# Performance work log

Measured on AMD Instinct MI355X. Metric: run time of the kernel, lower is better.

## Reference

```python
import jax, jax.numpy as jnp
import numpy as np

B, S, D = 4, 2048, 2048
H = 16
NOPE, ROPE, VD = 128, 64, 128
QK = NOPE + ROPE            # 192 per-head q/k dim
KVR = 512                   # kv_lora_rank
THETA = 10000.0
EPS = 1e-6
SCALE = QK ** -0.5


def _freqs(seq_len, d, theta):
    inv = 1.0 / (theta ** (np.arange(0, d, 2, dtype=np.float64) / d))
    ang = np.outer(np.arange(seq_len, dtype=np.float64), inv)  # [S, d//2]
    return jnp.asarray(np.cos(ang), jnp.float32), jnp.asarray(np.sin(ang), jnp.float32)


def apply_rope(x, cos, sin):
    # x: [B, S, H, d]; cos/sin: [S, d//2]; complex multiply on (even, odd) pairs
    xr = x.reshape(*x.shape[:-1], -1, 2)
    xe, xo = xr[..., 0], xr[..., 1]
    c = cos[None, :, None, :]
    s = sin[None, :, None, :]
    ye = xe * c - xo * s
    yo = xe * s + xo * c
    return jnp.stack([ye, yo], axis=-1).reshape(x.shape)


def rmsnorm(x, w, eps=EPS):
    return x * jax.lax.rsqrt(jnp.mean(x * x, axis=-1, keepdims=True) + eps) * w


def setup_inputs() -> dict:
    key = jax.random.key(0)
    ks = jax.random.split(key, 6)
    sd = 0.02
    x = jax.random.normal(ks[0], (B, S, D), jnp.float32)
    wq = jax.random.normal(ks[1], (H * QK, D), jnp.float32) * sd
    wkv_a = jax.random.normal(ks[2], (KVR + ROPE, D), jnp.float32) * sd
    kv_norm_w = jnp.ones((KVR,), jnp.float32)
    wkv_b = jax.random.normal(ks[3], (H * (NOPE + VD), KVR), jnp.float32) * sd
    wo = jax.random.normal(ks[4], (D, H * VD), jnp.float32) * sd
    cos, sin = _freqs(S, ROPE, THETA)
    return {"x": x, "wq": wq, "wkv_a": wkv_a, "kv_norm_w": kv_norm_w,
            "wkv_b": wkv_b, "wo": wo, "freqs_cos": cos, "freqs_sin": sin}


def reference(x, wq, wkv_a, kv_norm_w, wkv_b, wo, freqs_cos, freqs_sin):
    b, s, _ = x.shape
    # query projection (q_lora_rank == 0 path)
    q = jnp.einsum('bsd,ed->bse', x, wq).reshape(b, s, H, QK)
    q_nope, q_pe = q[..., :NOPE], q[..., NOPE:]
    q_pe = apply_rope(q_pe, freqs_cos, freqs_sin)

    # low-rank KV latent + decoupled rope key
    kv = jnp.einsum('bsd,ed->bse', x, wkv_a)          # [b,s,KVR+ROPE]
    kv_c, k_pe = kv[..., :KVR], kv[..., KVR:]
    k_pe = apply_rope(k_pe[:, :, None, :], freqs_cos, freqs_sin)  # [b,s,1,ROPE]
    kv_c = rmsnorm(kv_c, kv_norm_w)
    kvb = jnp.einsum('bsr,er->bse', kv_c, wkv_b).reshape(b, s, H, NOPE + VD)
    k_nope, v = kvb[..., :NOPE], kvb[..., NOPE:]
    k = jnp.concatenate([k_nope, jnp.broadcast_to(k_pe, (b, s, H, ROPE))], axis=-1)
    q_full = jnp.concatenate([q_nope, q_pe], axis=-1)

    # causal attention
    scores = jnp.einsum('bqhd,bkhd->bhqk', q_full, k) * SCALE
    mask = jnp.triu(jnp.full((s, s), -jnp.inf, jnp.float32), k=1)
    scores = scores + mask[None, None]
    p = jax.nn.softmax(scores, axis=-1)
    out = jnp.einsum('bhqk,bkhd->bqhd', p, v).reshape(b, s, H * VD)
    return jnp.einsum('bse,de->bsd', out, wo)
```

## Files before the change

### kernel.cpp

```cpp
#include <hip/hip_runtime.h>
#include <math.h>

#define BB 4
#define SS 2048
#define DD 2048
#define HH 16
#define NOPE 128
#define ROPE 64
#define VD 128
#define QKD 192
#define KVR 512
#define NP1 3712
#define ROWS (BB*SS)
#define SCL2 0.1041216338380858f

typedef __attribute__((ext_vector_type(8))) short bf16x8;
typedef __attribute__((ext_vector_type(4))) float f32x4;
typedef unsigned short bfu;
typedef __attribute__((address_space(1))) const void GV;
typedef __attribute__((address_space(3))) void LV;

__device__ __forceinline__ float bf2f(unsigned int u) {
    unsigned int i = u << 16; float f; __builtin_memcpy(&f, &i, 4); return f;
}
__device__ __forceinline__ unsigned int f2bf(float f) {
    unsigned int i; __builtin_memcpy(&i, &f, 4);
    return (i + 0x7fffu + ((i >> 16) & 1u)) >> 16;
}
__device__ __forceinline__ unsigned int cvt_pk_bf16(float lo, float hi) {
    unsigned int r;
    asm("v_cvt_pk_bf16_f32 %0, %1, %2" : "=v"(r) : "v"(lo), "v"(hi));
    return r;
}

__global__ void cast_f32_bf16(const float* __restrict__ src, bfu* __restrict__ dst,
                              long n_src, long n_dst) {
    long i = (long)blockIdx.x * blockDim.x + threadIdx.x;
    if (i * 4 >= n_dst) return;
    unsigned int lo = 0, hi = 0;
    if (i * 4 < n_src) {
        float4 v = ((const float4*)src)[i];
        lo = f2bf(v.x) | (f2bf(v.y) << 16);
        hi = f2bf(v.z) | (f2bf(v.w) << 16);
    }
    ((uint2*)dst)[i] = make_uint2(lo, hi);
}

__global__ void cast_weights(const float* __restrict__ wq, const float* __restrict__ wa,
                             const float* __restrict__ wb, const float* __restrict__ wo,
                             bfu* __restrict__ dq, bfu* __restrict__ da,
                             bfu* __restrict__ db, bfu* __restrict__ dwo) {
    long i = (long)blockIdx.x * 256 + threadIdx.x;
    const float* src; bfu* dst; long off, n_src; float scl = 1.0f;
    if (i < 1572864L)        { src = wq; dst = dq;  off = i;            n_src = 1572864L; scl = SCL2; }
    else if (i < 1900544L)   { src = wa; dst = da;  off = i - 1572864L; n_src = 294912L;  }
    else if (i < 2424832L)   { src = wb; dst = db;  off = i - 1900544L; n_src = 524288L;  }
    else if (i < 3473408L)   { src = wo; dst = dwo; off = i - 2424832L; n_src = 1048576L; }
    else return;
    unsigned int lo = 0, hi = 0;
    if (off < n_src) {
        float4 v = ((const float4*)src)[off];
        lo = f2bf(v.x * scl) | (f2bf(v.y * scl) << 16);
        hi = f2bf(v.z * scl) | (f2bf(v.w * scl) << 16);
    }
    ((uint2*)dst)[off] = make_uint2(lo, hi);
}

template <int MODE>
__global__ void __launch_bounds__(256)
gemm_bt(const bfu* __restrict__ A, const bfu* __restrict__ Bt,
        void* __restrict__ Cv, bfu* __restrict__ C2, int N, int K) {
    __shared__ __align__(16) char lds[32768];
    char* AsB = lds;
    char* BsB = lds + 16384;
    const int tid  = threadIdx.x;
    const int lane = tid & 63;
    const int wid  = tid >> 6;
    const int wr   = wid >> 1, wc = wid & 1;
    const long m0 = (long)blockIdx.y * 128;
    const long n0 = (long)blockIdx.x * 128;

    f32x4 acc[4][4] = {};

    const int lr = lane >> 3;
    const int SB = (lane & 7) << 4;

    for (int k0 = 0; k0 < K; k0 += 64) {
        __syncthreads();
#pragma unroll
        for (int i = 0; i < 4; ++i) {
            int rb = wid * 32 + i * 8;
            int R  = rb + lr;
            int c  = (SB ^ ((R & 7) << 4)) >> 1;
            const bfu* gA = A  + (m0 + R) * (long)K + k0 + c;
            const bfu* gB = Bt + (n0 + R) * (long)K + k0 + c;
            __builtin_amdgcn_global_load_lds((GV*)gA, (LV*)(AsB + rb * 128), 16, 0, 0);
            __builtin_amdgcn_global_load_lds((GV*)gB, (LV*)(BsB + rb * 128), 16, 0, 0);
        }
        __syncthreads();
#pragma unroll
        for (int kk = 0; kk < 2; ++kk) {
            bf16x8 av[4], bv[4];
            const int cb = kk * 64 + ((lane >> 4) << 4);
#pragma unroll
            for (int m = 0; m < 4; ++m) {
                int R = wr * 64 + m * 16 + (lane & 15);
                av[m] = *(const bf16x8*)(AsB + R * 128 + (cb ^ ((R & 7) << 4)));
            }
#pragma unroll
            for (int n = 0; n < 4; ++n) {
                int R = wc * 64 + n * 16 + (lane & 15);
                bv[n] = *(const bf16x8*)(BsB + R * 128 + (cb ^ ((R & 7) << 4)));
            }
#pragma unroll
            for (int m = 0; m < 4; ++m)
#pragma unroll
                for (int n = 0; n < 4; ++n)
                    acc[m][n] = __builtin_amdgcn_mfma_f32_16x16x32_bf16(av[m], bv[n], acc[m][n], 0, 0, 0);
        }
    }

    const int cr = (lane >> 4) << 2;
    const int cc = lane & 15;
#pragma unroll
    for (int m = 0; m < 4; ++m)
#pragma unroll
        for (int n = 0; n < 4; ++n)
#pragma unroll
            for (int r = 0; r < 4; ++r) {
                long row = m0 + wr * 64 + m * 16 + cr + r;
                long col = n0 + wc * 64 + n * 16 + cc;
                float val = acc[m][n][r];
                if (MODE == 1) {
                    ((float*)Cv)[row * N + col] = val;
                } else if (MODE == 0) {
                    ((bfu*)Cv)[row * N + col] = (bfu)f2bf(val);
                } else {
                    long b_ = row >> 11;
                    long s  = row & 2047;
                    long h  = col >> 8;
                    long wi = col & 255;
                    if (wi < 128)
                        C2[((b_ * HH + h) * SS + s) * (long)QKD + wi] = (bfu)f2bf(val);
                    else
                        ((bfu*)Cv)[row * 2048 + h * 128 + (wi - 128)] = (bfu)f2bf(val);
                }
            }
}

__global__ void rope_q(const bfu* __restrict__ p1, bfu* __restrict__ qr,
                       const float* __restrict__ fc, const float* __restrict__ fs) {
    long t = (long)blockIdx.x * 256 + threadIdx.x;
    int  ch = (int)(t % 24);
    long r  = t / 24;
    int  s  = (int)(r & 2047);
    long bh = r >> 11;
    long b_ = bh >> 4;
    int  h  = (int)(bh & 15);
    const bfu* src = p1 + (b_ * SS + s) * (long)NP1 + h * QKD + ch * 8;
    bfu* dst = qr + (bh * SS + s) * (long)QKD + ch * 8;
    bf16x8 v = *(const bf16x8*)src;
    if (ch >= 16) {
        int i0 = (ch - 16) * 4;
        unsigned int out[4];
#pragma unroll
        for (int k = 0; k < 4; ++k) {
            float e = bf2f((unsigned short)v[2 * k]);
            float o = bf2f((unsigned short)v[2 * k + 1]);
            float c = fc[s * 32 + i0 + k], sn = fs[s * 32 + i0 + k];
            out[k] = cvt_pk_bf16(e * c - o * sn, e * sn + o * c);
        }
        uint4 u = make_uint4(out[0], out[1], out[2], out[3]);
        *(uint4*)dst = u;
    } else {
        *(bf16x8*)dst = v;
    }
}

__global__ void __launch_bounds__(256)
rms_rope_kv(const bfu* __restrict__ p1, const float* __restrict__ wn,
            bfu* __restrict__ kvc, bfu* __restrict__ kpe,
            const float* __restrict__ fc, const float* __restrict__ fs) {
    const int row = blockIdx.x;
    const int t   = threadIdx.x;
    const int s   = row & (SS - 1);
    const long base = (long)row * NP1 + 3072;
    unsigned int v = *(const unsigned int*)(p1 + base + 2 * t);
    float a = bf2f(v & 0xffff), c2 = bf2f(v >> 16);
    float ssum = a * a + c2 * c2;
#pragma unroll
    for (int d = 1; d < 64; d <<= 1) ssum += __shfl_xor(ssum, d);
    __shared__ float red[4];
    const int lane = t & 63, w = t >> 6;
    if (lane == 0) red[w] = ssum;
    __syncthreads();
    float tot = red[0] + red[1] + red[2] + red[3];
    float scale = rsqrtf(tot * (1.0f / 512.0f) + 1e-6f);
    float w0 = wn[2 * t], w1 = wn[2 * t + 1];
    unsigned int out = f2bf(a * scale * w0) | (f2bf(c2 * scale * w1) << 16);
    *(unsigned int*)(kvc + (long)row * KVR + 2 * t) = out;
    if (t < 32) {
        unsigned int pv = *(const unsigned int*)(p1 + base + KVR + 2 * t);
        float e = bf2f(pv & 0xffff), o = bf2f(pv >> 16);
        float cc = fc[s * 32 + t], sn = fs[s * 32 + t];
        unsigned int po = f2bf(e * cc - o * sn) | (f2bf(e * sn + o * cc) << 16);
        *(unsigned int*)(kpe + (long)row * ROPE + 2 * t) = po;
    }
}

__global__ void pe_fill(const bfu* __restrict__ kpe, bfu* __restrict__ kall) {
    long t = (long)blockIdx.x * 256 + threadIdx.x;
    int  ch = (int)(t & 7);
    long r  = t >> 3;
    int  s  = (int)(r & 2047);
    long bh = r >> 11;
    long b_ = bh >> 4;
    bf16x8 v = *(const bf16x8*)(kpe + (b_ * SS + s) * (long)ROPE + ch * 8);
    *(bf16x8*)(kall + (bh * SS + s) * (long)QKD + NOPE + ch * 8) = v;
}

__global__ void __launch_bounds__(256)
transpose_v2(const bfu* __restrict__ vpack, bfu* __restrict__ vt) {
    __shared__ __align__(16) char tile[64 * 256];
    const int tid = threadIdx.x;
    const int bid = blockIdx.x;
    const int st  = bid & 31;
    const int bh  = bid >> 5;
    const int h   = bh & 15;
    const long b_ = bh >> 4;
    const long sbase = b_ * SS + st * 64;
#pragma unroll
    for (int i = 0; i < 4; ++i) {
        int idx = i * 256 + tid;
        int row = idx >> 4;
        int ch  = (idx & 15) ^ ((row >> 3) & 7);
        const bfu* src = vpack + (sbase + row) * 2048 + h * 128 + ch * 8;
        __builtin_amdgcn_global_load_lds((GV*)src, (LV*)(tile + idx * 16), 16, 0, 0);
    }
    __syncthreads();
#pragma unroll
    for (int i = 0; i < 4; ++i) {
        int idx = i * 256 + tid;
        int sc = idx & 7;
        int v  = (idx >> 3) & 127;
        bfu tmp[8];
#pragma unroll
        for (int k = 0; k < 8; ++k) {
            int row = sc * 8 + k;
            tmp[k] = *(const bfu*)(tile + row * 256 + (((v >> 3) ^ ((row >> 3) & 7)) << 4) + (v & 7) * 2);
        }
        *(bf16x8*)(vt + ((long)bh * VD + v) * SS + st * 64 + sc * 8) = *(bf16x8*)tmp;
    }
}

__device__ __forceinline__ void attn_tile64(
    const char* kbuf, const char* vbuf, char* pw,
    const bf16x8 (&qf)[6], f32x4 (&accv)[8],
    float& ms, float& ls, int kv0, int qa, int ql, int kg, int lane) {
    f32x4 sc[4] = {};
#pragma unroll
    for (int j = 0; j < 4; ++j)
#pragma unroll
        for (int d = 0; d < 6; ++d) {
            int row  = j * 16 + ql;
            int slot = (d * 4 + kg) ^ (ql & 7);
            bf16x8 kf = *(const bf16x8*)(kbuf + row * 384 + slot * 16);
            sc[j] = __builtin_amdgcn_mfma_f32_16x16x32_bf16(kf, qf[d], sc[j], 0, 0, 0);
        }
    float p[4][4];
    float mx = -1e30f;
#pragma unroll
    for (int j = 0; j < 4; ++j)
#pragma unroll
        for (int r = 0; r < 4; ++r) {
            float s = sc[j][r];
            int kv = kv0 + j * 16 + kg * 4 + r;
            s = (kv > qa) ? -1e30f : s;
            p[j][r] = s;
            mx = fmaxf(mx, s);
        }
    mx = fmaxf(mx, __shfl_xor(mx, 16));
    mx = fmaxf(mx, __shfl_xor(mx, 32));
    float rs = 0.f;
    if (__all(mx <= ms)) {
#pragma unroll
        for (int j = 0; j < 4; ++j)
#pragma unroll
            for (int r = 0; r < 4; ++r) {
                float e = exp2f(p[j][r] - ms);
                p[j][r] = e;
                rs += e;
            }
        rs += __shfl_xor(rs, 16);
        rs += __shfl_xor(rs, 32);
        ls += rs;
    } else {
        float mn = fmaxf(ms, mx);
        float al = exp2f(ms - mn);
        ms = mn;
#pragma unroll
        for (int j = 0; j < 4; ++j)
#pragma unroll
            for (int r = 0; r < 4; ++r) {
                float e = exp2f(p[j][r] - mn);
                p[j][r] = e;
                rs += e;
            }
        rs += __shfl_xor(rs, 16);
        rs += __shfl_xor(rs, 32);
        ls = ls * al + rs;
        float alT[4];
#pragma unroll
        for (int r = 0; r < 4; ++r)
            alT[r] = __shfl(al, (lane & 48) + kg * 4 + r);
#pragma unroll
        for (int v8 = 0; v8 < 8; ++v8)
#pragma unroll
            for (int r = 0; r < 4; ++r)
                accv[v8][r] *= alT[r];
    }
#pragma unroll
    for (int j = 0; j < 4; ++j) {
        uint2 u;
        u.x = cvt_pk_bf16(p[j][0], p[j][1]);
        u.y = cvt_pk_bf16(p[j][2], p[j][3]);
        int slot = (2 * j + (kg >> 1)) ^ (ql & 7);
        *(uint2*)(pw + ql * 128 + slot * 16 + (kg & 1) * 8) = u;
    }
    asm volatile("s_waitcnt lgkmcnt(0)" ::: "memory");
#pragma unroll
    for (int t2 = 0; t2 < 2; ++t2) {
        int ps = (t2 * 4 + kg) ^ (ql & 7);
        bf16x8 pa = *(const bf16x8*)(pw + ql * 128 + ps * 16);
#pragma unroll
        for (int v8 = 0; v8 < 8; ++v8) {
            int vrow = v8 * 16 + ql;
            int vs   = (t2 * 4 + kg) ^ (ql & 7);
            bf16x8 vf = *(const bf16x8*)(vbuf + vrow * 128 + vs * 16);
            accv[v8] = __builtin_amdgcn_mfma_f32_16x16x32_bf16(pa, vf, accv[v8], 0, 0, 0);
        }
    }
}

__global__ void __launch_bounds__(512)
attn(const bfu* __restrict__ qr, const bfu* __restrict__ kall,
     const bfu* __restrict__ vt, bfu* __restrict__ ao) {
    __shared__ __align__(16) char kbuf[64 * 384];
    __shared__ __align__(16) char vbuf[128 * 128];
    __shared__ __align__(16) char pbuf[8][2048];
    const int tid  = threadIdx.x;
    const int lane = tid & 63;
    const int w    = tid >> 6;
    const int ql   = lane & 15;
    const int kg   = lane >> 4;
    const int bid  = blockIdx.x;
    const int qb   = 15 - (bid >> 6);
    const int bh   = bid & 63;
    const int h    = bh & 15;
    const int b    = bh >> 4;
    const char* Q  = (const char*)(qr + (long)bh * SS * QKD);
    const char* Kp = (const char*)(kall + (long)bh * SS * QKD);
    const char* Vp = (const char*)(vt + (long)bh * VD * SS);
    char* pw = pbuf[w];

    const int qa_min = qb * 128 + w * 16;
    const int qa = qa_min + ql;

    bf16x8 qf[6];
#pragma unroll
    for (int d = 0; d < 6; ++d)
        qf[d] = *(const bf16x8*)(Q + (long)(qa_min + ql) * 384 + d * 64 + kg * 16);

    f32x4 accv[8] = {};
    float ms = -1e30f, ls = 0.f;
    const int ntiles = 2 * qb + 2;

    for (int t = 0; t < ntiles; ++t) {
        const int kv0 = t * 64;
        __syncthreads();
#pragma unroll
        for (int i = 0; i < 3; ++i) {
            int idx  = i * 512 + tid;
            int row  = idx / 24;
            int slot = idx - row * 24;
            int ss   = slot ^ (row & 7);
            const char* src = Kp + (long)(kv0 + row) * 384 + ss * 16;
            __builtin_amdgcn_global_load_lds((GV*)src, (LV*)(kbuf + idx * 16), 16, 0, 0);
        }
#pragma unroll
        for (int i = 0; i < 2; ++i) {
            int idx  = i * 512 + tid;
            int row  = idx >> 3;
            int slot = idx & 7;
            int ss   = slot ^ (row & 7);
            const char* src = Vp + (long)row * (SS * 2) + kv0 * 2 + ss * 16;
            __builtin_amdgcn_global_load_lds((GV*)src, (LV*)(vbuf + idx * 16), 16, 0, 0);
        }
        __syncthreads();
        if (kv0 <= qa_min + 15)
            attn_tile64(kbuf, vbuf, pw, qf, accv, ms, ls, kv0, qa, ql, kg, lane);
    }
    float li[4];
#pragma unroll
    for (int r = 0; r < 4; ++r)
        li[r] = 1.0f / __shfl(ls, (lane & 48) + kg * 4 + r);
#pragma unroll
    for (int v8 = 0; v8 < 8; ++v8)
#pragma unroll
        for (int r = 0; r < 4; ++r) {
            float o = accv[v8][r] * li[r];
            long row = (long)b * SS + qa_min + kg * 4 + r;
            ao[row * (long)(HH * VD) + h * VD + v8 * 16 + ql] = (bfu)f2bf(o);
        }
}

#define O_XB   0L
#define O_WQ   33554432L
#define O_WA   46137344L
#define O_WB   48758784L
#define O_WO   52953088L
#define O_P1   61341696L
#define O_QR   122159104L
#define O_KVC  172490752L
#define O_KPE  180879360L
#define O_AO   181927936L
#define WS_NEED 215482368L

extern "C" void kernel_launch(void* const* d_in, const int* in_sizes, int n_in,
                              void* d_out, int out_size, void* d_ws, size_t ws_size,
                              hipStream_t stream) {
    const float* x      = (const float*)d_in[0];
    const float* wq     = (const float*)d_in[1];
    const float* wkv_a  = (const float*)d_in[2];
    const float* kvnw   = (const float*)d_in[3];
    const float* wkv_b  = (const float*)d_in[4];
    const float* wo     = (const float*)d_in[5];
    const float* fcos   = (const float*)d_in[6];
    const float* fsin   = (const float*)d_in[7];
    if (ws_size < (size_t)WS_NEED) return;

    char* ws = (char*)d_ws;
    bfu* xb   = (bfu*)(ws + O_XB);
    bfu* wqb  = (bfu*)(ws + O_WQ);
    bfu* wab  = (bfu*)(ws + O_WA);
    bfu* wbb  = (bfu*)(ws + O_WB);
    bfu* wob  = (bfu*)(ws + O_WO);
    bfu* p1   = (bfu*)(ws + O_P1);
    bfu* qr   = (bfu*)(ws + O_QR);
    bfu* kvc  = (bfu*)(ws + O_KVC);
    bfu* kpe  = (bfu*)(ws + O_KPE);
    bfu* ao   = (bfu*)(ws + O_AO);
    bfu* kall = p1;
    bfu* vt   = xb;
    bfu* vpack = (bfu*)d_out;

    cast_f32_bf16<<<16384, 256, 0, stream>>>(x, xb, 16777216L, 16777216L);
    cast_weights<<<13568, 256, 0, stream>>>(wq, wkv_a, wkv_b, wo, wqb, wab, wbb, wob);

    gemm_bt<0><<<dim3(29, 64), 256, 0, stream>>>(xb, wqb, p1, nullptr, NP1, DD);

    rope_q<<<12288, 256, 0, stream>>>(p1, qr, fcos, fsin);
    rms_rope_kv<<<ROWS, 256, 0, stream>>>(p1, kvnw, kvc, kpe, fcos, fsin);

    gemm_bt<2><<<dim3(32, 64), 256, 0, stream>>>(kvc, wbb, vpack, kall, HH * 256, KVR);

    pe_fill<<<4096, 256, 0, stream>>>(kpe, kall);
    transpose_v2<<<2048, 256, 0, stream>>>(vpack, vt);

    attn<<<1024, 512, 0, stream>>>(qr, kall, vt, ao);

    gemm_bt<1><<<dim3(16, 64), 256, 0, stream>>>(ao, wob, d_out, nullptr, DD, HH * VD);
}
```

Measured before the change: 524.8 us.

## Double-buffer attention K/V tiles at 32-key granularity and swizzle GEMM block order

The attention loop moves from a single 64-key K/V buffer, loaded and then fully synchronised, to two 32-key buffers. The next tile's global-to-LDS loads are issued before the current tile is computed, with vmcnt waits and raw barriers in place of __syncthreads. Separately, the GEMM remaps its flat block index so that groups of neighbouring workgroups share A/B tiles in cache. The smaller tiles double the number of barriers and softmax rescale steps per query block. The vmcnt counts are hand-tuned and depend on how many loads each wave issues.

Result: slower. 569.9 us (+8.6%).

```diff
diff --git a/kernel.cpp b/kernel.cpp
--- a/kernel.cpp
+++ b/kernel.cpp
@@ -77,8 +77,11 @@
     const int lane = tid & 63;
     const int wid  = tid >> 6;
     const int wr   = wid >> 1, wc = wid & 1;
-    const long m0 = (long)blockIdx.y * 128;
-    const long n0 = (long)blockIdx.x * 128;
+    const int nwg  = gridDim.x * gridDim.y;
+    const int flat = blockIdx.y * gridDim.x + blockIdx.x;
+    const int swz  = (flat & 7) * (nwg >> 3) + (flat >> 3);
+    const long m0 = (long)(swz / gridDim.x) * 128;
+    const long n0 = (long)(swz % gridDim.x) * 128;
 
     f32x4 acc[4][4] = {};
 
@@ -253,24 +256,24 @@
     }
 }
 
-__device__ __forceinline__ void attn_tile64(
-    const char* kbuf, const char* vbuf, char* pw,
+__device__ __forceinline__ void attn_tile32(
+    const char* kb, const char* vb, char* pw,
     const bf16x8 (&qf)[6], f32x4 (&accv)[8],
     float& ms, float& ls, int kv0, int qa, int ql, int kg, int lane) {
-    f32x4 sc[4] = {};
-#pragma unroll
-    for (int j = 0; j < 4; ++j)
+    f32x4 sc[2] = {};
+#pragma unroll
+    for (int j = 0; j < 2; ++j)
 #pragma unroll
         for (int d = 0; d < 6; ++d) {
             int row  = j * 16 + ql;
             int slot = (d * 4 + kg) ^ (ql & 7);
-            bf16x8 kf = *(const bf16x8*)(kbuf + row * 384 + slot * 16);
+            bf16x8 kf = *(const bf16x8*)(kb + row * 384 + slot * 16);
             sc[j] = __builtin_amdgcn_mfma_f32_16x16x32_bf16(kf, qf[d], sc[j], 0, 0, 0);
         }
-    float p[4][4];
+    float p[2][4];
     float mx = -1e30f;
 #pragma unroll
-    for (int j = 0; j < 4; ++j)
+    for (int j = 0; j < 2; ++j)
 #pragma unroll
         for (int r = 0; r < 4; ++r) {
             float s = sc[j][r];
@@ -284,7 +287,7 @@
     float rs = 0.f;
     if (__all(mx <= ms)) {
 #pragma unroll
-        for (int j = 0; j < 4; ++j)
+        for (int j = 0; j < 2; ++j)
 #pragma unroll
             for (int r = 0; r < 4; ++r) {
                 float e = exp2f(p[j][r] - ms);
@@ -299,7 +302,7 @@
         float al = exp2f(ms - mn);
         ms = mn;
 #pragma unroll
-        for (int j = 0; j < 4; ++j)
+        for (int j = 0; j < 2; ++j)
 #pragma unroll
             for (int r = 0; r < 4; ++r) {
                 float e = exp2f(p[j][r] - mn);
@@ -320,34 +323,29 @@
                 accv[v8][r] *= alT[r];
     }
 #pragma unroll
-    for (int j = 0; j < 4; ++j) {
+    for (int j = 0; j < 2; ++j) {
         uint2 u;
         u.x = cvt_pk_bf16(p[j][0], p[j][1]);
         u.y = cvt_pk_bf16(p[j][2], p[j][3]);
-        int slot = (2 * j + (kg >> 1)) ^ (ql & 7);
-        *(uint2*)(pw + ql * 128 + slot * 16 + (kg & 1) * 8) = u;
+        int un = (j * 2 + (kg >> 1)) ^ (ql & 3);
+        *(uint2*)(pw + ql * 64 + un * 16 + (kg & 1) * 8) = u;
     }
     asm volatile("s_waitcnt lgkmcnt(0)" ::: "memory");
-#pragma unroll
-    for (int t2 = 0; t2 < 2; ++t2) {
-        int ps = (t2 * 4 + kg) ^ (ql & 7);
-        bf16x8 pa = *(const bf16x8*)(pw + ql * 128 + ps * 16);
-#pragma unroll
-        for (int v8 = 0; v8 < 8; ++v8) {
-            int vrow = v8 * 16 + ql;
-            int vs   = (t2 * 4 + kg) ^ (ql & 7);
-            bf16x8 vf = *(const bf16x8*)(vbuf + vrow * 128 + vs * 16);
-            accv[v8] = __builtin_amdgcn_mfma_f32_16x16x32_bf16(pa, vf, accv[v8], 0, 0, 0);
-        }
+    bf16x8 pa = *(const bf16x8*)(pw + ql * 64 + (kg ^ (ql & 3)) * 16);
+#pragma unroll
+    for (int v8 = 0; v8 < 8; ++v8) {
+        int vrow = v8 * 16 + ql;
+        bf16x8 vf = *(const bf16x8*)(vb + vrow * 64 + ((kg ^ (ql & 3)) << 4));
+        accv[v8] = __builtin_amdgcn_mfma_f32_16x16x32_bf16(pa, vf, accv[v8], 0, 0, 0);
     }
 }
 
 __global__ void __launch_bounds__(512)
 attn(const bfu* __restrict__ qr, const bfu* __restrict__ kall,
      const bfu* __restrict__ vt, bfu* __restrict__ ao) {
-    __shared__ __align__(16) char kbuf[64 * 384];
-    __shared__ __align__(16) char vbuf[128 * 128];
-    __shared__ __align__(16) char pbuf[8][2048];
+    __shared__ __align__(16) char kbuf[2][32 * 384];
+    __shared__ __align__(16) char vbuf[2][128 * 64];
+    __shared__ __align__(16) char pbuf[8][1024];
     const int tid  = threadIdx.x;
     const int lane = tid & 63;
     const int w    = tid >> 6;
@@ -365,6 +363,26 @@
 
     const int qa_min = qb * 128 + w * 16;
     const int qa = qa_min + ql;
+    const int tlast = (qa_min + 15) >> 5;
+
+    const int kr1 = tid / 24, ks1 = tid - kr1 * 24;
+    const char* kbase1 = Kp + kr1 * 384 + (ks1 ^ (kr1 & 7)) * 16;
+    const int kdst1 = tid * 16;
+    const int ki2 = 512 + tid;
+    const int kr2 = ki2 / 24, ks2 = ki2 - kr2 * 24;
+    const char* kbase2 = Kp + kr2 * 384 + (ks2 ^ (kr2 & 7)) * 16;
+    const int kdst2 = ki2 * 16;
+    const int vr = tid >> 2, vs = tid & 3;
+    const char* vbase = Vp + (long)vr * (SS * 2) + (vs ^ (vr & 3)) * 16;
+    const int vdst = tid * 16;
+    const bool second_k = (w < 4);
+
+    auto stage = [&](int bi, long kv0) {
+        __builtin_amdgcn_global_load_lds((GV*)(kbase1 + kv0 * 384), (LV*)(kbuf[bi] + kdst1), 16, 0, 0);
+        if (second_k)
+            __builtin_amdgcn_global_load_lds((GV*)(kbase2 + kv0 * 384), (LV*)(kbuf[bi] + kdst2), 16, 0, 0);
+        __builtin_amdgcn_global_load_lds((GV*)(vbase + kv0 * 2), (LV*)(vbuf[bi] + vdst), 16, 0, 0);
+    };
 
     bf16x8 qf[6];
 #pragma unroll
@@ -373,32 +391,25 @@
 
     f32x4 accv[8] = {};
     float ms = -1e30f, ls = 0.f;
-    const int ntiles = 2 * qb + 2;
-
+    const int ntiles = 4 * qb + 4;
+
+    stage(0, 0);
     for (int t = 0; t < ntiles; ++t) {
-        const int kv0 = t * 64;
-        __syncthreads();
-#pragma unroll
-        for (int i = 0; i < 3; ++i) {
-            int idx  = i * 512 + tid;
-            int row  = idx / 24;
-            int slot = idx - row * 24;
-            int ss   = slot ^ (row & 7);
-            const char* src = Kp + (long)(kv0 + row) * 384 + ss * 16;
-            __builtin_amdgcn_global_load_lds((GV*)src, (LV*)(kbuf + idx * 16), 16, 0, 0);
-        }
-#pragma unroll
-        for (int i = 0; i < 2; ++i) {
-            int idx  = i * 512 + tid;
-            int row  = idx >> 3;
-            int slot = idx & 7;
-            int ss   = slot ^ (row & 7);
-            const char* src = Vp + (long)row * (SS * 2) + kv0 * 2 + ss * 16;
-            __builtin_amdgcn_global_load_lds((GV*)src, (LV*)(vbuf + idx * 16), 16, 0, 0);
-        }
-        __syncthreads();
-        if (kv0 <= qa_min + 15)
-            attn_tile64(kbuf, vbuf, pw, qf, accv, ms, ls, kv0, qa, ql, kg, lane);
+        const int cur = t & 1;
+        const int kv0 = t * 32;
+        if (t + 1 < ntiles) {
+            stage(cur ^ 1, (long)(t + 1) * 32);
+            if (second_k) asm volatile("s_waitcnt vmcnt(3)" ::: "memory");
+            else          asm volatile("s_waitcnt vmcnt(2)" ::: "memory");
+        } else {
+            asm volatile("s_waitcnt vmcnt(0)" ::: "memory");
+        }
+        __builtin_amdgcn_s_barrier();
+        asm volatile("" ::: "memory");
+        if (t <= tlast)
+            attn_tile32(kbuf[cur], vbuf[cur], pw, qf, accv, ms, ls, kv0, qa, ql, kg, lane);
+        asm volatile("" ::: "memory");
+        __builtin_amdgcn_s_barrier();
     }
     float li[4];
 #pragma unroll
```
